# Kernel tuning notes

Hardware: AMD Instinct MI355X
Metric: run time of the kernel (lower is better)

Reference implementation:

```python
import jax, jax.numpy as jnp
import numpy as np

# NMS hyperparameters (from init_kwargs / standard detection settings)
CONF_THRESH = 0.05
NMS_THRESH = 0.5
MAX_PER_CLASS = 200
MAX_PER_IMAGE = 100
PRE_NMS_TOPK = 1000  # standard pre-NMS per-class candidate cap


def setup_inputs() -> dict:
    key = jax.random.key(0)
    k1, k2, k3 = jax.random.split(key, 3)
    N, C = 20000, 80
    # per-anchor per-class confidences in [0, 1]
    scores = jax.random.uniform(k1, (1, N, C), dtype=jnp.float32)
    # well-formed boxes (x1, y1, x2, y2) in normalized coords
    centers = jax.random.uniform(k2, (N, 2), dtype=jnp.float32)
    wh = jax.random.uniform(k3, (N, 2), dtype=jnp.float32) * 0.2 + 0.01
    boxes = jnp.concatenate([centers - wh / 2, centers + wh / 2], axis=-1)  # [N, 4]
    return {"scores": scores, "boxes": boxes}


def reference(scores, boxes):
    """Multiclass NMS: confidence threshold -> per-class greedy IoU suppression
    (max_per_class kept) -> global top-max_per_image. Returns kept scores
    (fixed shape [MAX_PER_IMAGE], zero-padded), matching the wrapper which
    returns the selected scores."""
    cls_scores_all = scores[0].T  # [C, N]
    j = jnp.arange(PRE_NMS_TOPK)

    def nms_one_class(cls_scores):  # [N] -> [MAX_PER_CLASS]
        top_s, idx = jax.lax.top_k(cls_scores, PRE_NMS_TOPK)  # [K]
        b = boxes[idx]  # [K, 4]
        x1, y1, x2, y2 = b[:, 0], b[:, 1], b[:, 2], b[:, 3]
        area = (x2 - x1) * (y2 - y1)  # [K]
        # pairwise IoU [K, K]
        iw = jnp.clip(jnp.minimum(x2[:, None], x2[None, :]) - jnp.maximum(x1[:, None], x1[None, :]), 0.0)
        ih = jnp.clip(jnp.minimum(y2[:, None], y2[None, :]) - jnp.maximum(y1[:, None], y1[None, :]), 0.0)
        inter = iw * ih
        iou = inter / (area[:, None] + area[None, :] - inter + 1e-9)
        valid = top_s > CONF_THRESH  # confidence threshold

        def body(i, keep):
            # if box i survives, suppress later boxes with IoU above threshold
            sup = keep[i] & (iou[i] > NMS_THRESH) & (j > i)
            return keep & ~sup

        keep = jax.lax.fori_loop(0, PRE_NMS_TOPK, body, valid)
        kept = jnp.where(keep, top_s, 0.0)
        return jax.lax.top_k(kept, MAX_PER_CLASS)[0]  # cap per class

    per_class = jax.vmap(nms_one_class)(cls_scores_all)  # [C, MAX_PER_CLASS]
    # global cap: top max_per_image scores across all classes
    return jax.lax.top_k(per_class.reshape(-1), MAX_PER_IMAGE)[0]
```

## Files before the change

kernel.cpp:

```cpp
#include <hip/hip_runtime.h>
#include <stdint.h>

#define N_DET 20000
#define N_CLS 80
#define NELEM (N_DET * N_CLS)
#define TOPK  1000
#define CONF  0.05f
#define CANDS 1280
#define SORTN 2048
#define FASTN 512
#define NBLK  128

typedef unsigned long long u64;
typedef unsigned int u32;

__device__ __forceinline__ bool iou_gt_half(float4 bi, float ai,
                                            float4 bj, float aj) {
  #pragma clang fp contract(off)
  float iw = fmaxf(fminf(bi.z, bj.z) - fmaxf(bi.x, bj.x), 0.0f);
  float ih = fmaxf(fminf(bi.w, bj.w) - fmaxf(bi.y, bj.y), 0.0f);
  float inter = iw * ih;
  float denom = ai + aj - inter + 1e-9f;
  return (double)inter * 33554432.0 > (double)denom * 16777217.0;
}

#define OFF_T16    0
#define OFF_T256   320
#define OFF_FLAG   640
#define OFF_CNT    960
#define OFF_CLSOUT 641280
#define OFF_GHA    682240
#define OFF_GHB    723200
#define OFF_CAND   805120
#define OFF_BCNT   1624320

__global__ __launch_bounds__(256) void k_zero(u32* __restrict__ gh) {
  uint4 z4 = make_uint4(0u, 0u, 0u, 0u);
  uint4* p = (uint4*)gh;
  int i = blockIdx.x * 256 + threadIdx.x;
  if (i < 7680) p[i] = z4;
}

__global__ __launch_bounds__(256) void k_histA(
    const float* __restrict__ S, u32* __restrict__ gh) {
  __shared__ u32 h[N_CLS * 129];
  for (int i = threadIdx.x; i < N_CLS * 129; i += 256) h[i] = 0;
  __syncthreads();
  const int per = NELEM / 4 / NBLK;
  const float4* S4 = (const float4*)S;
  const int v0 = blockIdx.x * per;
  for (int v = v0 + threadIdx.x; v < v0 + per; v += 256) {
    float4 f = S4[v];
    int c0 = (v * 4) % N_CLS;
    u32 b0 = __float_as_uint(f.x) >> 23; if (b0 > 127u) b0 = 127u;
    u32 b1 = __float_as_uint(f.y) >> 23; if (b1 > 127u) b1 = 127u;
    u32 b2 = __float_as_uint(f.z) >> 23; if (b2 > 127u) b2 = 127u;
    u32 b3 = __float_as_uint(f.w) >> 23; if (b3 > 127u) b3 = 127u;
    atomicAdd(&h[(c0 + 0) * 129 + b0], 1u);
    atomicAdd(&h[(c0 + 1) * 129 + b1], 1u);
    atomicAdd(&h[(c0 + 2) * 129 + b2], 1u);
    atomicAdd(&h[(c0 + 3) * 129 + b3], 1u);
  }
  __syncthreads();
  for (int i = threadIdx.x; i < N_CLS * 128; i += 256) {
    u32 v = h[(i >> 7) * 129 + (i & 127)];
    if (v) atomicAdd(&gh[i], v);
  }
}

__global__ __launch_bounds__(256) void k_histB_f(
    const float* __restrict__ S, const u32* __restrict__ ghA,
    u32* __restrict__ ghB) {
  __shared__ u32 h[N_CLS * 257];
  __shared__ u32 pA[N_CLS];
  for (int i = threadIdx.x; i < N_CLS * 128; i += 256)
    h[(i >> 7) * 129 + (i & 127)] = ghA[i];
  __syncthreads();
  if (threadIdx.x < N_CLS) {
    const int c = threadIdx.x;
    u32 acc = 0; u32 pref = 0;
    for (int b = 127; b >= 0; --b) {
      acc += h[c * 129 + b];
      if (acc >= TOPK) { pref = (u32)b; break; }
    }
    pA[c] = pref;
  }
  __syncthreads();
  for (int i = threadIdx.x; i < N_CLS * 257; i += 256) h[i] = 0;
  __syncthreads();
  const int per = NELEM / 4 / NBLK;
  const float4* S4 = (const float4*)S;
  const int v0 = blockIdx.x * per;
  for (int v = v0 + threadIdx.x; v < v0 + per; v += 256) {
    float4 f = S4[v];
    int c0 = (v * 4) % N_CLS;
    u32 bb[4] = {__float_as_uint(f.x), __float_as_uint(f.y),
                 __float_as_uint(f.z), __float_as_uint(f.w)};
    #pragma unroll
    for (int k = 0; k < 4; ++k) {
      u32 e = bb[k] >> 23; if (e > 127u) e = 127u;
      if (e == pA[c0 + k])
        atomicAdd(&h[(c0 + k) * 257 + ((bb[k] >> 15) & 0xFF)], 1u);
    }
  }
  __syncthreads();
  for (int i = threadIdx.x; i < N_CLS * 256; i += 256) {
    u32 v = h[(i >> 8) * 257 + (i & 255)];
    if (v) atomicAdd(&ghB[i], v);
  }
}

__global__ __launch_bounds__(256) void k_count_f(
    const float* __restrict__ S, const u32* __restrict__ ghA,
    const u32* __restrict__ ghB, u32* __restrict__ T16,
    u32* __restrict__ T256, u32* __restrict__ cnt, u32* __restrict__ bcnt) {
  __shared__ u32 hA[N_CLS * 129];
  __shared__ u32 hB[N_CLS * 257];
  __shared__ u32 tl[N_CLS];
  __shared__ u32 lcnt[N_CLS];
  for (int i = threadIdx.x; i < N_CLS * 128; i += 256)
    hA[(i >> 7) * 129 + (i & 127)] = ghA[i];
  for (int i = threadIdx.x; i < N_CLS * 256; i += 256)
    hB[(i >> 8) * 257 + (i & 255)] = ghB[i];
  for (int i = threadIdx.x; i < N_CLS; i += 256) lcnt[i] = 0;
  __syncthreads();
  if (threadIdx.x < N_CLS) {
    const int c = threadIdx.x;
    u32 acc = 0, pref = 0, tgt = TOPK, aboveA = 0;
    bool found = false;
    for (int b = 127; b >= 0; --b) {
      u32 hv = hA[c * 129 + b];
      acc += hv;
      if (acc >= TOPK) { pref = (u32)b; tgt = TOPK - (acc - hv);
                         aboveA = acc - hv; found = true; break; }
    }
    if (!found) { pref = 0; tgt = TOPK; aboveA = acc - hA[c * 129]; }
    u32 accB = 0, B1 = 0;
    for (int b = 255; b >= 0; --b) {
      accB += hB[c * 257 + b];
      if (accB >= tgt) { B1 = (u32)b; break; }
    }
    u32 t16 = (pref << 23) | (B1 << 15);
    tl[c] = t16;
    if (blockIdx.x == 0) {
      T16[c] = t16;
      cnt[c] = aboveA + accB;
      u32 t256 = t16;
      if (aboveA < 256u) {
        u32 rt = 256u - aboveA;
        u32 acc2 = 0, B2 = 0;
        for (int b = 255; b >= 0; --b) {
          acc2 += hB[c * 257 + b];
          if (acc2 >= rt) { B2 = (u32)b; break; }
        }
        t256 = (pref << 23) | (B2 << 15);
      }
      T256[c] = t256;
    }
  }
  __syncthreads();
  const int per = NELEM / 4 / NBLK;
  const float4* S4 = (const float4*)S;
  const int v0 = blockIdx.x * per;
  for (int v = v0 + threadIdx.x; v < v0 + per; v += 256) {
    float4 f = S4[v];
    const int c0 = (v * 4) % N_CLS;
    u32 bb[4] = {__float_as_uint(f.x), __float_as_uint(f.y),
                 __float_as_uint(f.z), __float_as_uint(f.w)};
    #pragma unroll
    for (int k = 0; k < 4; ++k)
      if (bb[k] >= tl[c0 + k]) atomicAdd(&lcnt[c0 + k], 1u);
  }
  __syncthreads();
  for (int i = threadIdx.x; i < N_CLS; i += 256)
    bcnt[blockIdx.x * N_CLS + i] = lcnt[i];
}

__global__ __launch_bounds__(256) void k_place_f(
    const float* __restrict__ S, const u32* __restrict__ T16,
    const u32* __restrict__ bcnt, u64* __restrict__ cand) {
  __shared__ u32 tl[N_CLS];
  __shared__ u32 lcnt[N_CLS];
  __shared__ u32 gbase[N_CLS];
  for (int i = threadIdx.x; i < N_CLS; i += 256) { tl[i] = T16[i]; lcnt[i] = 0; }
  if (threadIdx.x < N_CLS) {
    const int c = threadIdx.x;
    u32 a = 0;
    for (int b = 0; b < blockIdx.x; ++b) a += bcnt[b * N_CLS + c];
    gbase[c] = a;
  }
  __syncthreads();
  const int per = NELEM / 4 / NBLK;
  const float4* S4 = (const float4*)S;
  const int v0 = blockIdx.x * per;
  for (int v = v0 + threadIdx.x; v < v0 + per; v += 256) {
    float4 f = S4[v];
    const int base = v * 4;
    const int c0 = base % N_CLS;
    const u32 row = (u32)(base / N_CLS);
    u32 bb[4] = {__float_as_uint(f.x), __float_as_uint(f.y),
                 __float_as_uint(f.z), __float_as_uint(f.w)};
    #pragma unroll
    for (int k = 0; k < 4; ++k) {
      if (bb[k] >= tl[c0 + k]) {
        u32 p = gbase[c0 + k] + atomicAdd(&lcnt[c0 + k], 1u);
        if (p < CANDS)
          cand[(size_t)(c0 + k) * CANDS + p] = ((u64)bb[k] << 32) | (u32)(~row);
      }
    }
  }
}

__global__ __launch_bounds__(512) void k_sortnms(
    const u64* __restrict__ cand, const u32* __restrict__ cnt,
    const u32* __restrict__ T256, const float* __restrict__ boxes,
    float* __restrict__ cls_out, u32* __restrict__ flag) {
  const int c = blockIdx.x;
  const int tid = threadIdx.x, wave = tid >> 6, lane = tid & 63;
  __shared__ u64 keys[FASTN];
  __shared__ float4 sbox[FASTN];
  __shared__ float sarea[FASTN];
  __shared__ float sscore[FASTN];
  __shared__ u32 sN, sOvf;

  u32 n = cnt[c]; if (n > CANDS) n = CANDS;
  const u32 thr = T256[c];
  keys[tid] = 0ull;
  if (tid == 0) { sN = 0; sOvf = 0; }
  __syncthreads();
  for (int i = tid; i < (int)n; i += 512) {
    u64 kk = cand[(size_t)c * CANDS + i];
    if ((u32)(kk >> 32) >= thr) {
      u32 p = atomicAdd(&sN, 1u);
      if (p < FASTN) keys[p] = kk; else sOvf = 1u;
    }
  }
  __syncthreads();
  if (sOvf) { if (tid == 0) flag[c] = 1u; return; }
  const u32 nk = sN;

  const int segbase = wave * 64;
  for (int k = 2; k <= 64; k <<= 1) {
    for (int j = k >> 1; j > 0; j >>= 1) {
      if (lane < 32) {
        int p = lane;
        int i  = segbase + (((p & ~(j - 1)) << 1) | (p & (j - 1)));
        int ix = i | j;
        bool up = (i & k) == 0;
        u64 a = keys[i], b = keys[ix];
        if (up ? (a < b) : (a > b)) { keys[i] = b; keys[ix] = a; }
      }
      __builtin_amdgcn_wave_barrier();
    }
  }
  __syncthreads();
  for (int k = 128; k <= FASTN; k <<= 1) {
    for (int j = k >> 1; j >= 64; j >>= 1) {
      if (tid < 256) {
        int p = tid;
        int i  = ((p & ~(j - 1)) << 1) | (p & (j - 1));
        int ix = i | j;
        bool up = (i & k) == 0;
        u64 a = keys[i], b = keys[ix];
        if (up ? (a < b) : (a > b)) { keys[i] = b; keys[ix] = a; }
      }
      __syncthreads();
    }
    for (int j = 32; j > 0; j >>= 1) {
      if (lane < 32) {
        int p = lane;
        int i  = segbase + (((p & ~(j - 1)) << 1) | (p & (j - 1)));
        int ix = i | j;
        bool up = (i & k) == 0;
        u64 a = keys[i], b = keys[ix];
        if (up ? (a < b) : (a > b)) { keys[i] = b; keys[ix] = a; }
      }
      __builtin_amdgcn_wave_barrier();
    }
    __syncthreads();
  }

  {
    u64 kk = keys[tid];
    u32 idx = ~(u32)kk;
    if (kk == 0ull || idx >= N_DET) idx = 0;
    float4 b = ((const float4*)boxes)[idx];
    sbox[tid] = b;
    sarea[tid] = (b.z - b.x) * (b.w - b.y);
    sscore[tid] = __uint_as_float((u32)(kk >> 32));
  }
  __syncthreads();

  if (wave == 0) {
    float4 kb0 = make_float4(0.f, 0.f, 0.f, 0.f), kb1 = kb0;
    float ka0 = 0.f, ka1 = 0.f;
    int count = 0;
    bool confbreak = false;
    int ii = 0;
    float sc_n = sscore[0];
    float4 b_n = sbox[0];
    float a_n = sarea[0];
    for (; ii < FASTN && count < 100; ++ii) {
      float sc = sc_n;
      float4 bi = b_n;
      float ai = a_n;
      if (ii + 1 < FASTN) {
        sc_n = sscore[ii + 1];
        b_n = sbox[ii + 1];
        a_n = sarea[ii + 1];
      }
      if (!(sc > CONF)) { confbreak = true; break; }
      bool sup0 = (lane < count) && iou_gt_half(kb0, ka0, bi, ai);
      bool sup1 = (lane + 64 < count) && iou_gt_half(kb1, ka1, bi, ai);
      u64 m = __ballot(sup0 || sup1);
      if (m == 0ull) {
        if (count < 64) {
          if (lane == count) { kb0 = bi; ka0 = ai; }
        } else {
          if (lane == count - 64) { kb1 = bi; ka1 = ai; }
        }
        if (lane == 0) cls_out[c * 128 + count] = sc;
        ++count;
      }
    }
    bool done = (count >= 100) || (confbreak && ii < (int)nk);
    if (lane == 0) flag[c] = done ? 0u : 1u;
    if (done) {
      for (int i = count + lane; i < 100; i += 64)
        cls_out[c * 128 + i] = 0.0f;
    }
  }
}

__global__ __launch_bounds__(512) void k_nmsfull(
    const u64* __restrict__ cand, const u32* __restrict__ cnt,
    const u32* __restrict__ flag, const float* __restrict__ boxes,
    float* __restrict__ cls_out) {
  const int c = blockIdx.x;
  if (flag[c] == 0u) return;
  const int tid = threadIdx.x, wave = tid >> 6, lane = tid & 63;
  __shared__ u64 keys[SORTN];
  __shared__ float4 sbox[TOPK];
  __shared__ float sarea[TOPK];
  __shared__ float sscore[TOPK];

  u32 n = cnt[c]; if (n > CANDS) n = CANDS;
  for (int i = tid; i < SORTN; i += 512)
    keys[i] = (i < (int)n) ? cand[(size_t)c * CANDS + i] : 0ull;
  __syncthreads();
  const int segbase = wave * 256;
  for (int k = 2; k <= 256; k <<= 1) {
    for (int j = k >> 1; j > 0; j >>= 1) {
      #pragma unroll
      for (int q = 0; q < 2; ++q) {
        int p = lane + q * 64;
        int i  = segbase + (((p & ~(j - 1)) << 1) | (p & (j - 1)));
        int ix = i | j;
        bool up = (i & k) == 0;
        u64 a = keys[i], b = keys[ix];
        if (up ? (a < b) : (a > b)) { keys[i] = b; keys[ix] = a; }
      }
      __builtin_amdgcn_wave_barrier();
    }
  }
  __syncthreads();
  for (int k = 512; k <= SORTN; k <<= 1) {
    for (int j = k >> 1; j >= 256; j >>= 1) {
      for (int p = tid; p < SORTN / 2; p += 512) {
        int i  = ((p & ~(j - 1)) << 1) | (p & (j - 1));
        int ix = i | j;
        bool up = (i & k) == 0;
        u64 a = keys[i], b = keys[ix];
        if (up ? (a < b) : (a > b)) { keys[i] = b; keys[ix] = a; }
      }
      __syncthreads();
    }
    for (int j = 128; j > 0; j >>= 1) {
      #pragma unroll
      for (int q = 0; q < 2; ++q) {
        int p = lane + q * 64;
        int i  = segbase + (((p & ~(j - 1)) << 1) | (p & (j - 1)));
        int ix = i | j;
        bool up = (i & k) == 0;
        u64 a = keys[i], b = keys[ix];
        if (up ? (a < b) : (a > b)) { keys[i] = b; keys[ix] = a; }
      }
      __builtin_amdgcn_wave_barrier();
    }
    __syncthreads();
  }
  for (int i = tid; i < TOPK; i += 512) {
    u64 kk = keys[i];
    u32 idx = ~(u32)kk;
    if (kk == 0ull || idx >= N_DET) idx = 0;
    float4 b = ((const float4*)boxes)[idx];
    sbox[i] = b;
    sarea[i] = (b.z - b.x) * (b.w - b.y);
    sscore[i] = __uint_as_float((u32)(kk >> 32));
  }
  __syncthreads();
  if (wave == 0) {
    float4 kb0 = make_float4(0.f, 0.f, 0.f, 0.f), kb1 = kb0;
    float ka0 = 0.f, ka1 = 0.f;
    int count = 0;
    float sc_n = sscore[0];
    float4 b_n = sbox[0];
    float a_n = sarea[0];
    for (int i = 0; i < TOPK && count < 100; ++i) {
      float sc = sc_n;
      float4 bi = b_n;
      float ai = a_n;
      if (i + 1 < TOPK) {
        sc_n = sscore[i + 1];
        b_n = sbox[i + 1];
        a_n = sarea[i + 1];
      }
      if (!(sc > CONF)) break;
      bool sup0 = (lane < count) && iou_gt_half(kb0, ka0, bi, ai);
      bool sup1 = (lane + 64 < count) && iou_gt_half(kb1, ka1, bi, ai);
      u64 m = __ballot(sup0 || sup1);
      if (m == 0ull) {
        if (count < 64) {
          if (lane == count) { kb0 = bi; ka0 = ai; }
        } else {
          if (lane == count - 64) { kb1 = bi; ka1 = ai; }
        }
        if (lane == 0) cls_out[c * 128 + count] = sc;
        ++count;
      }
    }
    for (int i = count + lane; i < 100; i += 64)
      cls_out[c * 128 + i] = 0.0f;
  }
}

__global__ __launch_bounds__(1024) void k_final(
    const float* __restrict__ cls_out, float* __restrict__ out) {
  __shared__ u32 vals[8000];
  __shared__ u32 h1[8192];
  __shared__ u32 h2[16384];
  __shared__ u32 wsum[16];
  __shared__ u32 cands[512];
  __shared__ u32 sPref, sT2, sThr, scnt;
  const int t = threadIdx.x, wave = t >> 6, lane = t & 63;

  uint4 z4 = make_uint4(0u, 0u, 0u, 0u);
  for (int i = t; i < 2048; i += 1024) ((uint4*)h1)[i] = z4;
  for (int i = t; i < 4096; i += 1024) ((uint4*)h2)[i] = z4;
  if (t < 128) ((uint4*)cands)[t] = z4;
  if (t == 0) { sPref = 0; sT2 = 1; sThr = 0; scnt = 0; }
  __syncthreads();

  for (int i = t; i < 8000; i += 1024) {
    u32 b = __float_as_uint(cls_out[(i / 100) * 128 + (i % 100)]);
    vals[i] = b;
    u32 bin = b >> 17; if (bin > 8191u) bin = 8191u;
    atomicAdd(&h1[bin], 1u);
  }
  __syncthreads();

  {
    const u32 b0 = (u32)t * 8u;
    u32 loc[8]; u32 lsum = 0;
    #pragma unroll
    for (int k = 0; k < 8; ++k) { loc[k] = h1[b0 + k]; lsum += loc[k]; }
    u32 s = lsum;
    #pragma unroll
    for (int off = 1; off < 64; off <<= 1) {
      u32 v = __shfl_down(s, off, 64);
      if (lane + off < 64) s += v;
    }
    if (lane == 0) wsum[wave] = s;
    __syncthreads();
    u32 aboveW = 0;
    #pragma unroll
    for (int w = 0; w < 16; ++w) if (w > wave) aboveW += wsum[w];
    u32 above = aboveW + (s - lsum);
    if (above < 100u && above + lsum >= 100u) {
      u32 acc = above;
      #pragma unroll
      for (int k = 7; k >= 0; --k) {
        acc += loc[k];
        if (acc >= 100u) { sPref = b0 + (u32)k; sT2 = 100u - (acc - loc[k]); break; }
      }
    }
    __syncthreads();
  }
  const u32 pref = sPref, rt = sT2;

  for (int i = t; i < 8000; i += 1024) {
    u32 b = vals[i];
    u32 bin = b >> 17; if (bin > 8191u) bin = 8191u;
    if (bin == pref) atomicAdd(&h2[(b >> 3) & 0x3FFFu], 1u);
  }
  __syncthreads();

  {
    const u32 b0 = (u32)t * 16u;
    u32 loc[16]; u32 lsum = 0;
    #pragma unroll
    for (int k = 0; k < 16; ++k) { loc[k] = h2[b0 + k]; lsum += loc[k]; }
    u32 s = lsum;
    #pragma unroll
    for (int off = 1; off < 64; off <<= 1) {
      u32 v = __shfl_down(s, off, 64);
      if (lane + off < 64) s += v;
    }
    if (lane == 0) wsum[wave] = s;
    __syncthreads();
    u32 aboveW = 0;
    #pragma unroll
    for (int w = 0; w < 16; ++w) if (w > wave) aboveW += wsum[w];
    u32 above = aboveW + (s - lsum);
    if (above < rt && above + lsum >= rt) {
      u32 acc = above;
      #pragma unroll
      for (int k = 15; k >= 0; --k) {
        acc += loc[k];
        if (acc >= rt) { sThr = (pref << 17) | ((b0 + (u32)k) << 3); break; }
      }
    }
    __syncthreads();
  }
  const u32 thr = sThr;

  for (int i = t; i < 8000; i += 1024) {
    u32 v = vals[i];
    if (v >= thr) {
      u32 p = atomicAdd(&scnt, 1u);
      if (p < 512u) cands[p] = v;
    }
  }
  __syncthreads();
  const u32 nc = scnt;

  if (nc <= 512u) {
    if (wave == 0) {
      for (int k = 2; k <= 512; k <<= 1)
        for (int j = k >> 1; j > 0; j >>= 1) {
          for (int p = lane; p < 256; p += 64) {
            int i  = ((p & ~(j - 1)) << 1) | (p & (j - 1));
            int ix = i | j;
            bool up = (i & k) == 0;
            u32 a = cands[i], b = cands[ix];
            if (up ? (a < b) : (a > b)) { cands[i] = b; cands[ix] = a; }
          }
          __builtin_amdgcn_wave_barrier();
        }
      out[lane] = __uint_as_float(cands[lane]);
      if (lane < 36) out[lane + 64] = __uint_as_float(cands[lane + 64]);
    }
  } else {
    for (int i = t; i < 8192; i += 1024) h2[i] = (i < 8000) ? vals[i] : 0u;
    __syncthreads();
    for (int k = 2; k <= 8192; k <<= 1)
      for (int j = k >> 1; j > 0; j >>= 1) {
        for (int p = t; p < 4096; p += 1024) {
          int i  = ((p & ~(j - 1)) << 1) | (p & (j - 1));
          int ix = i | j;
          bool up = (i & k) == 0;
          u32 a = h2[i], b = h2[ix];
          if (up ? (a < b) : (a > b)) { h2[i] = b; h2[ix] = a; }
        }
        __syncthreads();
      }
    if (t < 100) out[t] = __uint_as_float(h2[t]);
  }
}

extern "C" void kernel_launch(void* const* d_in, const int* in_sizes, int n_in,
                              void* d_out, int out_size, void* d_ws, size_t ws_size,
                              hipStream_t stream) {
  const float* scores = (const float*)d_in[0];
  const float* boxes  = (const float*)d_in[1];
  float* out = (float*)d_out;
  char* ws = (char*)d_ws;

  u32* T16     = (u32*)(ws + OFF_T16);
  u32* T256    = (u32*)(ws + OFF_T256);
  u32* flag    = (u32*)(ws + OFF_FLAG);
  u32* cnt     = (u32*)(ws + OFF_CNT);
  float* cls_out = (float*)(ws + OFF_CLSOUT);
  u32* ghistA  = (u32*)(ws + OFF_GHA);
  u32* ghistB  = (u32*)(ws + OFF_GHB);
  u64* cand    = (u64*)(ws + OFF_CAND);
  u32* bcnt    = (u32*)(ws + OFF_BCNT);

  k_zero<<<30, 256, 0, stream>>>(ghistA);
  k_histA<<<NBLK, 256, 0, stream>>>(scores, ghistA);
  k_histB_f<<<NBLK, 256, 0, stream>>>(scores, ghistA, ghistB);
  k_count_f<<<NBLK, 256, 0, stream>>>(scores, ghistA, ghistB, T16, T256, cnt, bcnt);
  k_place_f<<<NBLK, 256, 0, stream>>>(scores, T16, bcnt, cand);
  k_sortnms<<<N_CLS, 512, 0, stream>>>(cand, cnt, T256, boxes, cls_out, flag);
  k_nmsfull<<<N_CLS, 512, 0, stream>>>(cand, cnt, flag, boxes, cls_out);
  k_final<<<1, 1024, 0, stream>>>(cls_out, out);
}
```

Measured before the change: 146.0 us.

## Merge fast-path and full NMS kernels into one block; shrink fast path

Folds the fallback full-sort NMS kernel into the fast-path kernel, so a block that cannot finish from its small candidate set falls through to the full 2048-key sort in-kernel. This removes one kernel launch and the flag round-trip through global memory. The fast-path candidate set drops from 512 to 256 (threshold at rank 160) and blocks go from 512 to 256 threads. In exchange, the fallback sort runs with half the threads, and the block now reserves the full 2048-key and 1000-box shared arrays, which may lower occupancy.

```diff
diff --git a/kernel.cpp b/kernel.cpp
--- a/kernel.cpp
+++ b/kernel.cpp
@@ -8,7 +8,7 @@
 #define CONF  0.05f
 #define CANDS 1280
 #define SORTN 2048
-#define FASTN 512
+#define FASTN 256
 #define NBLK  128
 
 typedef unsigned long long u64;
@@ -25,8 +25,7 @@
 }
 
 #define OFF_T16    0
-#define OFF_T256   320
-#define OFF_FLAG   640
+#define OFF_T160   320
 #define OFF_CNT    960
 #define OFF_CLSOUT 641280
 #define OFF_GHA    682240
@@ -113,7 +112,7 @@
 __global__ __launch_bounds__(256) void k_count_f(
     const float* __restrict__ S, const u32* __restrict__ ghA,
     const u32* __restrict__ ghB, u32* __restrict__ T16,
-    u32* __restrict__ T256, u32* __restrict__ cnt, u32* __restrict__ bcnt) {
+    u32* __restrict__ T160, u32* __restrict__ cnt, u32* __restrict__ bcnt) {
   __shared__ u32 hA[N_CLS * 129];
   __shared__ u32 hB[N_CLS * 257];
   __shared__ u32 tl[N_CLS];
@@ -145,17 +144,17 @@
     if (blockIdx.x == 0) {
       T16[c] = t16;
       cnt[c] = aboveA + accB;
-      u32 t256 = t16;
-      if (aboveA < 256u) {
-        u32 rt = 256u - aboveA;
+      u32 t160 = t16;
+      if (aboveA < 160u) {
+        u32 rt = 160u - aboveA;
         u32 acc2 = 0, B2 = 0;
         for (int b = 255; b >= 0; --b) {
           acc2 += hB[c * 257 + b];
           if (acc2 >= rt) { B2 = (u32)b; break; }
         }
-        t256 = (pref << 23) | (B2 << 15);
-      }
-      T256[c] = t256;
+        t160 = (pref << 23) | (B2 << 15);
+      }
+      T160[c] = t160;
     }
   }
   __syncthreads();
@@ -211,24 +210,24 @@
   }
 }
 
-__global__ __launch_bounds__(512) void k_sortnms(
+__global__ __launch_bounds__(256) void k_sortnms(
     const u64* __restrict__ cand, const u32* __restrict__ cnt,
-    const u32* __restrict__ T256, const float* __restrict__ boxes,
-    float* __restrict__ cls_out, u32* __restrict__ flag) {
+    const u32* __restrict__ T160, const float* __restrict__ boxes,
+    float* __restrict__ cls_out) {
   const int c = blockIdx.x;
   const int tid = threadIdx.x, wave = tid >> 6, lane = tid & 63;
-  __shared__ u64 keys[FASTN];
-  __shared__ float4 sbox[FASTN];
-  __shared__ float sarea[FASTN];
-  __shared__ float sscore[FASTN];
-  __shared__ u32 sN, sOvf;
+  __shared__ u64 keys[SORTN];
+  __shared__ float4 sbox[TOPK];
+  __shared__ float sarea[TOPK];
+  __shared__ float sscore[TOPK];
+  __shared__ u32 sN, sOvf, sDone;
 
   u32 n = cnt[c]; if (n > CANDS) n = CANDS;
-  const u32 thr = T256[c];
+  const u32 thr = T160[c];
   keys[tid] = 0ull;
-  if (tid == 0) { sN = 0; sOvf = 0; }
-  __syncthreads();
-  for (int i = tid; i < (int)n; i += 512) {
+  if (tid == 0) { sN = 0; sOvf = 0; sDone = 0; }
+  __syncthreads();
+  for (int i = tid; i < (int)n; i += 256) {
     u64 kk = cand[(size_t)c * CANDS + i];
     if ((u32)(kk >> 32) >= thr) {
       u32 p = atomicAdd(&sN, 1u);
@@ -236,15 +235,114 @@
     }
   }
   __syncthreads();
-  if (sOvf) { if (tid == 0) flag[c] = 1u; return; }
   const u32 nk = sN;
 
-  const int segbase = wave * 64;
-  for (int k = 2; k <= 64; k <<= 1) {
+  if (!sOvf) {
+    const int segbase = wave * 64;
+    for (int k = 2; k <= 64; k <<= 1) {
+      for (int j = k >> 1; j > 0; j >>= 1) {
+        if (lane < 32) {
+          int p = lane;
+          int i  = segbase + (((p & ~(j - 1)) << 1) | (p & (j - 1)));
+          int ix = i | j;
+          bool up = (i & k) == 0;
+          u64 a = keys[i], b = keys[ix];
+          if (up ? (a < b) : (a > b)) { keys[i] = b; keys[ix] = a; }
+        }
+        __builtin_amdgcn_wave_barrier();
+      }
+    }
+    __syncthreads();
+    for (int k = 128; k <= FASTN; k <<= 1) {
+      for (int j = k >> 1; j >= 64; j >>= 1) {
+        if (tid < 128) {
+          int p = tid;
+          int i  = ((p & ~(j - 1)) << 1) | (p & (j - 1));
+          int ix = i | j;
+          bool up = (i & k) == 0;
+          u64 a = keys[i], b = keys[ix];
+          if (up ? (a < b) : (a > b)) { keys[i] = b; keys[ix] = a; }
+        }
+        __syncthreads();
+      }
+      for (int j = 32; j > 0; j >>= 1) {
+        if (lane < 32) {
+          int p = lane;
+          int i  = segbase + (((p & ~(j - 1)) << 1) | (p & (j - 1)));
+          int ix = i | j;
+          bool up = (i & k) == 0;
+          u64 a = keys[i], b = keys[ix];
+          if (up ? (a < b) : (a > b)) { keys[i] = b; keys[ix] = a; }
+        }
+        __builtin_amdgcn_wave_barrier();
+      }
+      __syncthreads();
+    }
+
+    {
+      u64 kk = keys[tid];
+      u32 idx = ~(u32)kk;
+      if (kk == 0ull || idx >= N_DET) idx = 0;
+      float4 b = ((const float4*)boxes)[idx];
+      sbox[tid] = b;
+      sarea[tid] = (b.z - b.x) * (b.w - b.y);
+      sscore[tid] = __uint_as_float((u32)(kk >> 32));
+    }
+    __syncthreads();
+
+    if (wave == 0) {
+      float4 kb0 = make_float4(0.f, 0.f, 0.f, 0.f), kb1 = kb0;
+      float ka0 = 0.f, ka1 = 0.f;
+      int count = 0;
+      bool confbreak = false;
+      int ii = 0;
+      float sc_n = sscore[0];
+      float4 b_n = sbox[0];
+      float a_n = sarea[0];
+      for (; ii < FASTN && count < 100; ++ii) {
+        float sc = sc_n;
+        float4 bi = b_n;
+        float ai = a_n;
+        if (ii + 1 < FASTN) {
+          sc_n = sscore[ii + 1];
+          b_n = sbox[ii + 1];
+          a_n = sarea[ii + 1];
+        }
+        if (!(sc > CONF)) { confbreak = true; break; }
+        bool sup0 = (lane < count) && iou_gt_half(kb0, ka0, bi, ai);
+        bool sup1 = (lane + 64 < count) && iou_gt_half(kb1, ka1, bi, ai);
+        u64 m = __ballot(sup0 || sup1);
+        if (m == 0ull) {
+          if (count < 64) {
+            if (lane == count) { kb0 = bi; ka0 = ai; }
+          } else {
+            if (lane == count - 64) { kb1 = bi; ka1 = ai; }
+          }
+          if (lane == 0) cls_out[c * 128 + count] = sc;
+          ++count;
+        }
+      }
+      bool done = (count >= 100) || (confbreak && ii < (int)nk);
+      if (lane == 0) sDone = done ? 1u : 0u;
+      if (done) {
+        for (int i = count + lane; i < 100; i += 64)
+          cls_out[c * 128 + i] = 0.0f;
+      }
+    }
+  }
+  __syncthreads();
+  if (sDone) return;
+
+  for (int i = tid; i < SORTN; i += 256)
+    keys[i] = (i < (int)n) ? cand[(size_t)c * CANDS + i] : 0ull;
+  __syncthreads();
+  const int seg2 = wave * 512;
+  for (int k = 2; k <= 512; k <<= 1) {
     for (int j = k >> 1; j > 0; j >>= 1) {
-      if (lane < 32) {
-        int p = lane;
-        int i  = segbase + (((p & ~(j - 1)) << 1) | (p & (j - 1)));
+      #pragma unroll
+      for (int q = 0; q < 4; ++q) {
+        int p = lane + q * 64;
+        int i  = seg2 + (((p & ~(j - 1)) << 1) | (p & (j - 1)));
         int ix = i | j;
         bool up = (i & k) == 0;
         u64 a = keys[i], b = keys[ix];
@@ -254,10 +352,9 @@
     }
   }
   __syncthreads();
-  for (int k = 128; k <= FASTN; k <<= 1) {
-    for (int j = k >> 1; j >= 64; j >>= 1) {
-      if (tid < 256) {
-        int p = tid;
+  for (int k = 1024; k <= SORTN; k <<= 1) {
+    for (int j = k >> 1; j >= 512; j >>= 1) {
+      for (int p = tid; p < SORTN / 2; p += 256) {
         int i  = ((p & ~(j - 1)) << 1) | (p & (j - 1));
         int ix = i | j;
         bool up = (i & k) == 0;
@@ -266,10 +363,11 @@
       }
       __syncthreads();
     }
-    for (int j = 32; j > 0; j >>= 1) {
-      if (lane < 32) {
-        int p = lane;
-        int i  = segbase + (((p & ~(j - 1)) << 1) | (p & (j - 1)));
+    for (int j = 256; j > 0; j >>= 1) {
+      #pragma unroll
+      for (int q = 0; q < 4; ++q) {
+        int p = lane + q * 64;
+        int i  = seg2 + (((p & ~(j - 1)) << 1) | (p & (j - 1)));
         int ix = i | j;
         bool up = (i & k) == 0;
         u64 a = keys[i], b = keys[ix];
@@ -279,117 +377,7 @@
     }
     __syncthreads();
   }
-
-  {
-    u64 kk = keys[tid];
-    u32 idx = ~(u32)kk;
-    if (kk == 0ull || idx >= N_DET) idx = 0;
-    float4 b = ((const float4*)boxes)[idx];
-    sbox[tid] = b;
-    sarea[tid] = (b.z - b.x) * (b.w - b.y);
-    sscore[tid] = __uint_as_float((u32)(kk >> 32));
-  }
-  __syncthreads();
-
-  if (wave == 0) {
-    float4 kb0 = make_float4(0.f, 0.f, 0.f, 0.f), kb1 = kb0;
-    float ka0 = 0.f, ka1 = 0.f;
-    int count = 0;
-    bool confbreak = false;
-    int ii = 0;
-    float sc_n = sscore[0];
-    float4 b_n = sbox[0];
-    float a_n = sarea[0];
-    for (; ii < FASTN && count < 100; ++ii) {
-      float sc = sc_n;
-      float4 bi = b_n;
-      float ai = a_n;
-      if (ii + 1 < FASTN) {
-        sc_n = sscore[ii + 1];
-        b_n = sbox[ii + 1];
-        a_n = sarea[ii + 1];
-      }
-      if (!(sc > CONF)) { confbreak = true; break; }
-      bool sup0 = (lane < count) && iou_gt_half(kb0, ka0, bi, ai);
-      bool sup1 = (lane + 64 < count) && iou_gt_half(kb1, ka1, bi, ai);
-      u64 m = __ballot(sup0 || sup1);
-      if (m == 0ull) {
-        if (count < 64) {
-          if (lane == count) { kb0 = bi; ka0 = ai; }
-        } else {
-          if (lane == count - 64) { kb1 = bi; ka1 = ai; }
-        }
-        if (lane == 0) cls_out[c * 128 + count] = sc;
-        ++count;
-      }
-    }
-    bool done = (count >= 100) || (confbreak && ii < (int)nk);
-    if (lane == 0) flag[c] = done ? 0u : 1u;
-    if (done) {
-      for (int i = count + lane; i < 100; i += 64)
-        cls_out[c * 128 + i] = 0.0f;
-    }
-  }
-}
-
-__global__ __launch_bounds__(512) void k_nmsfull(
-    const u64* __restrict__ cand, const u32* __restrict__ cnt,
-    const u32* __restrict__ flag, const float* __restrict__ boxes,
-    float* __restrict__ cls_out) {
-  const int c = blockIdx.x;
-  if (flag[c] == 0u) return;
-  const int tid = threadIdx.x, wave = tid >> 6, lane = tid & 63;
-  __shared__ u64 keys[SORTN];
-  __shared__ float4 sbox[TOPK];
-  __shared__ float sarea[TOPK];
-  __shared__ float sscore[TOPK];
-
-  u32 n = cnt[c]; if (n > CANDS) n = CANDS;
-  for (int i = tid; i < SORTN; i += 512)
-    keys[i] = (i < (int)n) ? cand[(size_t)c * CANDS + i] : 0ull;
-  __syncthreads();
-  const int segbase = wave * 256;
-  for (int k = 2; k <= 256; k <<= 1) {
-    for (int j = k >> 1; j > 0; j >>= 1) {
-      #pragma unroll
-      for (int q = 0; q < 2; ++q) {
-        int p = lane + q * 64;
-        int i  = segbase + (((p & ~(j - 1)) << 1) | (p & (j - 1)));
-        int ix = i | j;
-        bool up = (i & k) == 0;
-        u64 a = keys[i], b = keys[ix];
-        if (up ? (a < b) : (a > b)) { keys[i] = b; keys[ix] = a; }
-      }
-      __builtin_amdgcn_wave_barrier();
-    }
-  }
-  __syncthreads();
-  for (int k = 512; k <= SORTN; k <<= 1) {
-    for (int j = k >> 1; j >= 256; j >>= 1) {
-      for (int p = tid; p < SORTN / 2; p += 512) {
-        int i  = ((p & ~(j - 1)) << 1) | (p & (j - 1));
-        int ix = i | j;
-        bool up = (i & k) == 0;
-        u64 a = keys[i], b = keys[ix];
-        if (up ? (a < b) : (a > b)) { keys[i] = b; keys[ix] = a; }
-      }
-      __syncthreads();
-    }
-    for (int j = 128; j > 0; j >>= 1) {
-      #pragma unroll
-      for (int q = 0; q < 2; ++q) {
-        int p = lane + q * 64;
-        int i  = segbase + (((p & ~(j - 1)) << 1) | (p & (j - 1)));
-        int ix = i | j;
-        bool up = (i & k) == 0;
-        u64 a = keys[i], b = keys[ix];
-        if (up ? (a < b) : (a > b)) { keys[i] = b; keys[ix] = a; }
-      }
-      __builtin_amdgcn_wave_barrier();
-    }
-    __syncthreads();
-  }
-  for (int i = tid; i < TOPK; i += 512) {
+  for (int i = tid; i < TOPK; i += 256) {
     u64 kk = keys[i];
     u32 idx = ~(u32)kk;
     if (kk == 0ull || idx >= N_DET) idx = 0;
@@ -577,8 +565,7 @@
   char* ws = (char*)d_ws;
 
   u32* T16     = (u32*)(ws + OFF_T16);
-  u32* T256    = (u32*)(ws + OFF_T256);
-  u32* flag    = (u32*)(ws + OFF_FLAG);
+  u32* T160    = (u32*)(ws + OFF_T160);
   u32* cnt     = (u32*)(ws + OFF_CNT);
   float* cls_out = (float*)(ws + OFF_CLSOUT);
   u32* ghistA  = (u32*)(ws + OFF_GHA);
@@ -589,9 +576,8 @@
   k_zero<<<30, 256, 0, stream>>>(ghistA);
   k_histA<<<NBLK, 256, 0, stream>>>(scores, ghistA);
   k_histB_f<<<NBLK, 256, 0, stream>>>(scores, ghistA, ghistB);
-  k_count_f<<<NBLK, 256, 0, stream>>>(scores, ghistA, ghistB, T16, T256, cnt, bcnt);
+  k_count_f<<<NBLK, 256, 0, stream>>>(scores, ghistA, ghistB, T16, T160, cnt, bcnt);
   k_place_f<<<NBLK, 256, 0, stream>>>(scores, T16, bcnt, cand);
-  k_sortnms<<<N_CLS, 512, 0, stream>>>(cand, cnt, T256, boxes, cls_out, flag);
-  k_nmsfull<<<N_CLS, 512, 0, stream>>>(cand, cnt, flag, boxes, cls_out);
+  k_sortnms<<<N_CLS, 256, 0, stream>>>(cand, cnt, T160, boxes, cls_out);
   k_final<<<1, 1024, 0, stream>>>(cls_out, out);
 }
```

Result: no change. 143.8 us, median of 2 (-1.5%).
